# Kernel optimization log

Hardware: AMD Instinct MI355X
Metric: run time of the kernel (lower is better)

Reference implementation:

```python
import jax, jax.numpy as jnp
import numpy as np

HIDDEN = 2048
NUM_HEADS = 16
HEAD_DIM = HIDDEN // NUM_HEADS


def setup_inputs() -> dict:
    key = jax.random.key(0)
    k1, k2, k3 = jax.random.split(key, 3)
    B, S = 2, 2048
    hidden_states = jax.random.normal(k1, (B, S, HIDDEN), dtype=jnp.float32)
    attention_mask = jnp.zeros((B, 1, 1, S), dtype=jnp.float32)
    W_qkv = jax.random.normal(k2, (HIDDEN, 3 * HIDDEN), dtype=jnp.float32) * (1.0 / np.sqrt(HIDDEN))
    b_qkv = jnp.zeros((3 * HIDDEN,), dtype=jnp.float32)
    W_out = jax.random.normal(k3, (HIDDEN, HIDDEN), dtype=jnp.float32) * (1.0 / np.sqrt(HIDDEN))
    b_out = jnp.zeros((HIDDEN,), dtype=jnp.float32)
    return {"hidden_states": hidden_states, "attention_mask": attention_mask,
            "W_qkv": W_qkv, "b_qkv": b_qkv, "W_out": W_out, "b_out": b_out}


def reference(hidden_states, attention_mask, W_qkv, b_qkv, W_out, b_out):
    B, S, H = hidden_states.shape
    scale = 1.0 / np.sqrt(HEAD_DIM)
    # fused QKV projection (column-parallel linear, world_size=1)
    mixed = hidden_states @ W_qkv + b_qkv                      # [B,S,3H]
    q, k, v = jnp.split(mixed, 3, axis=-1)
    # [B, heads, S, head_dim]
    q = q.reshape(B, S, NUM_HEADS, HEAD_DIM).transpose(0, 2, 1, 3)
    k = k.reshape(B, S, NUM_HEADS, HEAD_DIM).transpose(0, 2, 1, 3)
    v = v.reshape(B, S, NUM_HEADS, HEAD_DIM).transpose(0, 2, 1, 3)
    scores = jnp.einsum('bhqd,bhkd->bhqk', q, k) * scale       # [B,h,S,S]
    scores = scores + attention_mask                            # additive mask broadcast
    probs = jax.nn.softmax(scores, axis=-1)
    ctx = jnp.einsum('bhqk,bhkd->bhqd', probs, v)               # [B,h,S,d]
    ctx = ctx.transpose(0, 2, 1, 3).reshape(B, S, H)
    return ctx @ W_out + b_out
```

## Files before the change

kernel.cpp:

```cpp
#include <hip/hip_runtime.h>
#include <hip/hip_bf16.h>
#include <stdint.h>

typedef __attribute__((ext_vector_type(4))) float   f32x4;
typedef __attribute__((ext_vector_type(8))) __bf16  bf16x8;
typedef __attribute__((ext_vector_type(4))) __bf16  bf16x4;
typedef __attribute__((ext_vector_type(8))) short   s16x8;
typedef __attribute__((ext_vector_type(4))) unsigned short u16x4;
typedef __attribute__((ext_vector_type(4))) float   fl4;

#define DEVFN static __device__ __forceinline__

constexpr int BATCH = 2, SEQ = 2048, HID = 2048, NHEAD = 16, HDIM = 128;
constexpr int MROWS = BATCH * SEQ;
constexpr int N3    = 3 * HID;
constexpr float LOG2E = 1.44269504088896340736f;
constexpr float SCALE_LOG2E = 0.12751649736170852f;
constexpr float DEFER_THR = 11.541560327111708f;

DEVFN unsigned short f2bf(float f) {
  unsigned int u = __float_as_uint(f);
  u += 0x7FFFu + ((u >> 16) & 1u);
  return (unsigned short)(u >> 16);
}
DEVFN float bf2f(unsigned short h) { return __uint_as_float(((unsigned int)h) << 16); }

DEVFN void async_cp16(const void* g, void* l) {
  __builtin_amdgcn_global_load_lds(
      (__attribute__((address_space(1))) void*)g,
      (__attribute__((address_space(3))) void*)l, 16, 0, 0);
}

DEVFN f32x4 mfma_bf16(bf16x8 a, bf16x8 b, f32x4 c) {
  return __builtin_amdgcn_mfma_f32_16x16x32_bf16(a, b, c, 0, 0, 0);
}

__global__ __launch_bounds__(256) void cvt_bf16(const float* __restrict__ x,
                                                unsigned short* __restrict__ hi, int n4) {
  for (int i = blockIdx.x * blockDim.x + threadIdx.x; i < n4; i += gridDim.x * blockDim.x) {
    fl4 v = ((const fl4*)x)[i];
    u16x4 h;
#pragma unroll
    for (int j = 0; j < 4; j++) h[j] = f2bf(v[j]);
    ((u16x4*)hi)[i] = h;
  }
}

__global__ __launch_bounds__(256) void cvt_transpose(const float* __restrict__ W,
                                                     unsigned short* __restrict__ T,
                                                     int R, int C) {
  __shared__ float tile[32][33];
  const int c0 = blockIdx.x * 32, r0 = blockIdx.y * 32;
  const int tx = threadIdx.x, ty = threadIdx.y;
#pragma unroll
  for (int i = 0; i < 4; i++) tile[ty + 8 * i][tx] = W[(size_t)(r0 + ty + 8 * i) * C + c0 + tx];
  __syncthreads();
#pragma unroll
  for (int i = 0; i < 4; i++) {
    const float v = tile[tx][ty + 8 * i];
    T[(size_t)(c0 + ty + 8 * i) * R + r0 + tx] = f2bf(v);
  }
}

template <bool OUT_BF16>
__global__ __launch_bounds__(512, 1) void gemm_ring(const unsigned short* __restrict__ A,
                                                    const unsigned short* __restrict__ Bt,
                                                    const float* __restrict__ bias,
                                                    void* __restrict__ Cout, int Ndim) {
  constexpr int KDIM  = 2048;
  constexpr int NT    = KDIM / 64;
  constexpr int ASLOT = 256 * 64;
  constexpr int BSLOT = 128 * 64;
  constexpr int SLOT  = ASLOT + BSLOT;
  __shared__ __align__(16) unsigned short smem[3 * SLOT];

  const int tid = threadIdx.x;
  const int wid = tid >> 6, lane = tid & 63;
  const int wm = wid >> 2, wn = wid & 3;
  const int g = lane >> 4, q = lane & 15;
  const int n0 = blockIdx.x * 128, m0 = blockIdx.y * 256;

  const int srow = (wid << 3) + (lane >> 3);
  const int scol = (((lane & 7) ^ (lane >> 3)) << 4);
  const char* gA = (const char*)A  + ((size_t)(m0 + srow) * KDIM) * 2 + scol;
  const char* gB = (const char*)Bt + ((size_t)(n0 + srow) * KDIM) * 2 + scol;
  const int dbase = ((wid << 3)) << 7;

  f32x4 acc[8][2] = {};
  const int axor = (q & 7) << 4;

  auto STAGE = [&](int tt, int slot) {
    char* sA = (char*)(smem + slot * SLOT);
    char* sB = (char*)(smem + slot * SLOT + ASLOT);
    const size_t koff = (size_t)tt << 7;
#pragma unroll
    for (int i = 0; i < 4; i++)
      async_cp16(gA + (size_t)(i * 64) * (KDIM * 2) + koff, sA + dbase + (i << 13));
#pragma unroll
    for (int i = 0; i < 2; i++)
      async_cp16(gB + (size_t)(i * 64) * (KDIM * 2) + koff, sB + dbase + (i << 13));
  };

  auto COMPUTE = [&](int slot) {
    const char* sA = (const char*)(smem + slot * SLOT);
    const char* sB = (const char*)(smem + slot * SLOT + ASLOT);
#pragma unroll
    for (int ks = 0; ks < 2; ks++) {
      const int kb = (ks << 6) + (g << 4);
      bf16x8 av[8], bv[2];
#pragma unroll
      for (int nf = 0; nf < 2; nf++) {
        const int row = (wn << 5) + (nf << 4) + q;
        bv[nf] = *(const bf16x8*)(sB + (row << 7) + (kb ^ axor));
      }
#pragma unroll
      for (int mf = 0; mf < 8; mf++) {
        const int row = (wm << 7) + (mf << 4) + q;
        av[mf] = *(const bf16x8*)(sA + (row << 7) + (kb ^ axor));
      }
#pragma unroll
      for (int mf = 0; mf < 8; mf++)
#pragma unroll
        for (int nf = 0; nf < 2; nf++)
          acc[mf][nf] = mfma_bf16(av[mf], bv[nf], acc[mf][nf]);
    }
  };

  STAGE(0, 0);
  STAGE(1, 1);
  int s2 = 2, sc = 0;
#pragma unroll 1
  for (int t = 0; t < NT - 2; ++t) {
    asm volatile("s_waitcnt vmcnt(6)" ::: "memory");
    __builtin_amdgcn_s_barrier();
    asm volatile("" ::: "memory");
    STAGE(t + 2, s2);
    COMPUTE(sc);
    s2 = (s2 == 2) ? 0 : s2 + 1;
    sc = (sc == 2) ? 0 : sc + 1;
  }
  asm volatile("s_waitcnt vmcnt(6)" ::: "memory");
  __builtin_amdgcn_s_barrier();
  asm volatile("" ::: "memory");
  COMPUTE(sc);
  sc = (sc == 2) ? 0 : sc + 1;
  asm volatile("s_waitcnt vmcnt(0)" ::: "memory");
  __builtin_amdgcn_s_barrier();
  asm volatile("" ::: "memory");
  COMPUTE(sc);

  float bvv[2];
#pragma unroll
  for (int nf = 0; nf < 2; nf++) bvv[nf] = bias[n0 + (wn << 5) + (nf << 4) + q];
#pragma unroll
  for (int mf = 0; mf < 8; mf++) {
    const int rowg = m0 + (wm << 7) + (mf << 4) + (g << 2);
#pragma unroll
    for (int nf = 0; nf < 2; nf++) {
      const int colg = n0 + (wn << 5) + (nf << 4) + q;
#pragma unroll
      for (int r = 0; r < 4; r++) {
        const float v = acc[mf][nf][r] + bvv[nf];
        if (OUT_BF16)
          ((unsigned short*)Cout)[(size_t)(rowg + r) * Ndim + colg] = f2bf(v);
        else
          ((float*)Cout)[(size_t)(rowg + r) * Ndim + colg] = v;
      }
    }
  }
}

__global__ __launch_bounds__(256) void transpose_v(const unsigned short* __restrict__ qkv,
                                                   unsigned short* __restrict__ vt) {
  __shared__ __align__(16) unsigned short tile[64][136];
  const int z = blockIdx.y, b = z >> 4, h = z & 15;
  const int s0 = blockIdx.x << 6;
  const int t = threadIdx.x;
#pragma unroll
  for (int i = 0; i < 4; i++) {
    const int idx = t + (i << 8);
    const int row = idx >> 4, ch = idx & 15;
    *(s16x8*)&tile[row][ch << 3] =
        *(const s16x8*)(qkv + (size_t)(b * SEQ + s0 + row) * N3 + 2 * HID + h * HDIM + (ch << 3));
  }
  __syncthreads();
#pragma unroll
  for (int i = 0; i < 4; i++) {
    const int idx = t + (i << 8);
    const int d = idx >> 3, sc = idx & 7;
    s16x8 v;
#pragma unroll
    for (int j = 0; j < 8; j++) v[j] = (short)tile[(sc << 3) + j][d];
    *(s16x8*)(vt + (size_t)(z * HDIM + d) * SEQ + s0 + (sc << 3)) = v;
  }
}

__global__ __launch_bounds__(512, 2) void attn_kernel(const unsigned short* __restrict__ qkv,
                                                      const unsigned short* __restrict__ vt,
                                                      const float* __restrict__ mask,
                                                      unsigned short* __restrict__ ctx) {
  constexpr int NT    = SEQ / 64;
  constexpr int KSLOT = 64 * 128;
  constexpr int VSLOT = 128 * 64;
  constexpr int SLOT  = KSLOT + VSLOT;
  __shared__ __align__(16) unsigned short sKV[3 * SLOT];
  __shared__ __align__(16) unsigned short sP[8][32 * 72];
  __shared__ __align__(16) float sM[SEQ];

  const int bid = blockIdx.x;
  const int z  = ((bid & 7) << 2) + ((bid >> 3) >> 3);
  const int qb = (bid >> 3) & 7;
  const int b = z >> 4, h = z & 15;
  const int tid = threadIdx.x, wid = tid >> 6, lane = tid & 63;
  const int g = lane >> 4, q = lane & 15;
  const int q0 = (qb << 8) + (wid << 5);

  {
    fl4 m = ((const fl4*)(mask + (size_t)b * SEQ))[tid];
    m *= LOG2E;
    ((fl4*)sM)[tid] = m;
  }

  bf16x8 bq[2][4];
#pragma unroll
  for (int qs = 0; qs < 2; qs++) {
    const unsigned short* qrow = qkv + (size_t)(b * SEQ + q0 + (qs << 4) + q) * N3 + h * HDIM;
#pragma unroll
    for (int c = 0; c < 4; c++) bq[qs][c] = *(const bf16x8*)(qrow + (c << 5) + (g << 3));
  }

  f32x4 acc[2][8] = {};
  float mrun[2] = {-1e30f, -1e30f}, lrun[2] = {0.f, 0.f};
  unsigned short* myP = &sP[wid][0];
  const int sbase = (lane & 48) | (g << 2);

  const char* gK = (const char*)qkv + ((size_t)(b * SEQ) * N3 + HID + h * HDIM) * 2;
  const char* gV = (const char*)vt + ((size_t)z * HDIM * SEQ) * 2;

  auto STAGE = [&](int tt, int slot) {
    char* base = (char*)(sKV + slot * SLOT);
    const int k0 = tt << 6;
#pragma unroll
    for (int i = 0; i < 2; i++) {
      const int krow = (i << 5) + (tid >> 4);
      const int kc = (((tid & 15) << 4)) ^ ((krow & 7) << 4);
      async_cp16(gK + ((size_t)(k0 + krow) * N3) * 2 + kc, base + (i << 13) + (wid << 10));
    }
#pragma unroll
    for (int i = 0; i < 2; i++) {
      const int vrow = (i << 6) + (tid >> 3);
      const int vc = (((tid & 7) << 4)) ^ ((vrow & 7) << 4);
      async_cp16(gV + ((size_t)vrow * SEQ + k0) * 2 + vc,
                 base + (KSLOT * 2) + (i << 13) + (wid << 10));
    }
  };

  auto COMPUTE = [&](int t, int slot) {
    const char* sK = (const char*)(sKV + slot * SLOT);
    const char* sV = (const char*)(sKV + slot * SLOT + KSLOT);
    const int k0 = t << 6;

    f32x4 accs[2][4];
#pragma unroll
    for (int qs = 0; qs < 2; qs++)
#pragma unroll
      for (int kt = 0; kt < 4; kt++) accs[qs][kt] = (f32x4){0.f, 0.f, 0.f, 0.f};
#pragma unroll
    for (int c = 0; c < 4; c++) {
      const int kbyte = (c << 6) + (g << 4);
#pragma unroll
      for (int kt = 0; kt < 4; kt++) {
        const int key = (kt << 4) + q;
        const bf16x8 ak = *(const bf16x8*)(sK + (key << 8) + (kbyte ^ ((key & 7) << 4)));
        accs[0][kt] = mfma_bf16(ak, bq[0][c], accs[0][kt]);
        accs[1][kt] = mfma_bf16(ak, bq[1][c], accs[1][kt]);
      }
    }

    fl4 mk2[4];
#pragma unroll
    for (int kt = 0; kt < 4; kt++) mk2[kt] = *(const fl4*)&sM[k0 + (kt << 4) + (g << 2)];

#pragma unroll
    for (int qs = 0; qs < 2; qs++) {
      float s2[4][4];
      float km[4];
#pragma unroll
      for (int kt = 0; kt < 4; kt++) {
#pragma unroll
        for (int r = 0; r < 4; r++)
          s2[kt][r] = fmaf(accs[qs][kt][r], SCALE_LOG2E, mk2[kt][r]);
        km[kt] = fmaxf(fmaxf(s2[kt][0], s2[kt][1]), fmaxf(s2[kt][2], s2[kt][3]));
      }
      float mt = fmaxf(fmaxf(km[0], km[1]), fmaxf(km[2], km[3]));
      mt = fmaxf(mt, __shfl_xor(mt, 16));
      mt = fmaxf(mt, __shfl_xor(mt, 32));
      if (!__all(mt <= mrun[qs] + DEFER_THR)) {
        const float mnew = fmaxf(mrun[qs], mt);
        const float fs = exp2f(mrun[qs] - mnew);
        lrun[qs] *= fs;
#pragma unroll
        for (int r = 0; r < 4; r++) {
          const float fr = __shfl(fs, sbase + r);
#pragma unroll
          for (int dt = 0; dt < 8; dt++) acc[qs][dt][r] *= fr;
        }
        mrun[qs] = mnew;
      }
      float pst[4];
#pragma unroll
      for (int kt = 0; kt < 4; kt++) {
        bf16x4 pk;
        float e0 = exp2f(s2[kt][0] - mrun[qs]);
        float e1 = exp2f(s2[kt][1] - mrun[qs]);
        float e2 = exp2f(s2[kt][2] - mrun[qs]);
        float e3 = exp2f(s2[kt][3] - mrun[qs]);
        pk[0] = (__bf16)e0; pk[1] = (__bf16)e1; pk[2] = (__bf16)e2; pk[3] = (__bf16)e3;
        pst[kt] = (e0 + e1) + (e2 + e3);
        *(bf16x4*)((char*)myP + ((qs << 4) + q) * 144 + (((kt << 4) + (g << 2)) << 1)) = pk;
      }
      float ps = (pst[0] + pst[1]) + (pst[2] + pst[3]);
      ps += __shfl_xor(ps, 16);
      ps += __shfl_xor(ps, 32);
      lrun[qs] += ps;
    }

    asm volatile("s_waitcnt lgkmcnt(0)" ::: "memory");
    __builtin_amdgcn_sched_barrier(0);

#pragma unroll
    for (int kc = 0; kc < 2; kc++) {
      const bf16x8 pa0 = *(const bf16x8*)((const char*)myP + q * 144 + (kc << 6) + (g << 4));
      const bf16x8 pa1 = *(const bf16x8*)((const char*)myP + (16 + q) * 144 + (kc << 6) + (g << 4));
      const int kbyte = (kc << 6) + (g << 4);
#pragma unroll
      for (int dt = 0; dt < 8; dt++) {
        const int d = (dt << 4) + q;
        const bf16x8 bvv = *(const bf16x8*)(sV + (d << 7) + (kbyte ^ ((d & 7) << 4)));
        acc[0][dt] = mfma_bf16(pa0, bvv, acc[0][dt]);
        acc[1][dt] = mfma_bf16(pa1, bvv, acc[1][dt]);
      }
    }
  };

  STAGE(0, 0);
  STAGE(1, 1);
  __syncthreads();
  int s2 = 2, sc = 0;
#pragma unroll 1
  for (int t = 0; t < NT - 2; ++t) {
    asm volatile("s_waitcnt vmcnt(4)" ::: "memory");
    __builtin_amdgcn_s_barrier();
    asm volatile("" ::: "memory");
    STAGE(t + 2, s2);
    COMPUTE(t, sc);
    s2 = (s2 == 2) ? 0 : s2 + 1;
    sc = (sc == 2) ? 0 : sc + 1;
  }
  asm volatile("s_waitcnt vmcnt(4)" ::: "memory");
  __builtin_amdgcn_s_barrier();
  asm volatile("" ::: "memory");
  COMPUTE(NT - 2, sc);
  sc = (sc == 2) ? 0 : sc + 1;
  asm volatile("s_waitcnt vmcnt(0)" ::: "memory");
  __builtin_amdgcn_s_barrier();
  asm volatile("" ::: "memory");
  COMPUTE(NT - 1, sc);

#pragma unroll
  for (int qs = 0; qs < 2; qs++)
#pragma unroll
    for (int r = 0; r < 4; r++) {
      const float lr = __shfl(lrun[qs], sbase + r);
      const float inv = 1.f / lr;
      const int token = b * SEQ + q0 + (qs << 4) + (g << 2) + r;
      unsigned short* crow = ctx + (size_t)token * HID + h * HDIM + q;
#pragma unroll
      for (int dt = 0; dt < 8; dt++) crow[dt << 4] = f2bf(acc[qs][dt][r] * inv);
    }
}

extern "C" void kernel_launch(void* const* d_in, const int* in_sizes, int n_in,
                              void* d_out, int out_size, void* d_ws, size_t ws_size,
                              hipStream_t stream) {
  const float* hs   = (const float*)d_in[0];
  const float* mask = (const float*)d_in[1];
  const float* Wqkv = (const float*)d_in[2];
  const float* bqkv = (const float*)d_in[3];
  const float* Wout = (const float*)d_in[4];
  const float* bout = (const float*)d_in[5];

  char* ws = (char*)d_ws;
  size_t off = 0;
  auto alloc = [&](size_t n) { char* p = ws + off; off += (n + 255) & ~(size_t)255; return p; };
  unsigned short* hs_bf = (unsigned short*)alloc((size_t)MROWS * HID * 2);
  unsigned short* wq_bf = (unsigned short*)alloc((size_t)N3 * HID * 2);
  unsigned short* wo_bf = (unsigned short*)alloc((size_t)HID * HID * 2);
  unsigned short* qkvb  = (unsigned short*)alloc((size_t)MROWS * N3 * 2);
  unsigned short* vtb   = (unsigned short*)alloc((size_t)BATCH * NHEAD * HDIM * SEQ * 2);
  unsigned short* ctxb  = (unsigned short*)alloc((size_t)MROWS * HID * 2);
  (void)ws_size;

  cvt_bf16<<<2048, 256, 0, stream>>>(hs, hs_bf, MROWS * HID / 4);
  dim3 tb(32, 8);
  cvt_transpose<<<dim3(N3 / 32, HID / 32), tb, 0, stream>>>(Wqkv, wq_bf, HID, N3);
  cvt_transpose<<<dim3(HID / 32, HID / 32), tb, 0, stream>>>(Wout, wo_bf, HID, HID);
  gemm_ring<true ><<<dim3(N3 / 128, MROWS / 256), 512, 0, stream>>>(hs_bf, wq_bf, bqkv, qkvb, N3);
  transpose_v<<<dim3(SEQ / 64, BATCH * NHEAD), 256, 0, stream>>>(qkvb, vtb);
  attn_kernel<<<256, 512, 0, stream>>>(qkvb, vtb, mask, ctxb);
  gemm_ring<false><<<dim3(HID / 128, MROWS / 256), 512, 0, stream>>>(ctxb, wo_bf, bout, (float*)d_out, HID);
}
```

Measured before the change: 272.6 us.

## Switch attention to 32x32x16 MFMA with in-register P via permlane32 swap

Rewrites the attention inner loop to use 32x32x16 bf16 MFMA tiles, so each wave computes S^T for 32 queries by 32 keys and accumulates the output with 32-wide tiles. The probability matrix is packed with v_cvt_pk_bf16 and rearranged across lane halves using permlane32_swap, which removes the per-wave shared-memory P buffer and its LDS round trip and wait. It also raises wave priority around the MFMA blocks. This reduces LDS traffic and instruction count, at the cost of a more intricate register layout and possible register pressure at two waves per SIMD.

Result: no change. 268.9 us (-1.3%).

```diff
diff --git a/kernel.cpp b/kernel.cpp
--- a/kernel.cpp
+++ b/kernel.cpp
@@ -2,12 +2,14 @@
 #include <hip/hip_bf16.h>
 #include <stdint.h>
 
-typedef __attribute__((ext_vector_type(4))) float   f32x4;
-typedef __attribute__((ext_vector_type(8))) __bf16  bf16x8;
-typedef __attribute__((ext_vector_type(4))) __bf16  bf16x4;
-typedef __attribute__((ext_vector_type(8))) short   s16x8;
-typedef __attribute__((ext_vector_type(4))) unsigned short u16x4;
-typedef __attribute__((ext_vector_type(4))) float   fl4;
+typedef __attribute__((ext_vector_type(4)))  float   f32x4;
+typedef __attribute__((ext_vector_type(16))) float   f32x16;
+typedef __attribute__((ext_vector_type(8)))  __bf16  bf16x8;
+typedef __attribute__((ext_vector_type(8)))  short   s16x8;
+typedef __attribute__((ext_vector_type(4)))  unsigned short u16x4;
+typedef __attribute__((ext_vector_type(4)))  float   fl4;
+typedef __attribute__((ext_vector_type(2)))  unsigned int u32x2;
+typedef __attribute__((ext_vector_type(4)))  unsigned int u32x4;
 
 #define DEVFN static __device__ __forceinline__
 
@@ -33,6 +35,14 @@
 
 DEVFN f32x4 mfma_bf16(bf16x8 a, bf16x8 b, f32x4 c) {
   return __builtin_amdgcn_mfma_f32_16x16x32_bf16(a, b, c, 0, 0, 0);
+}
+DEVFN f32x16 mfma32(bf16x8 a, bf16x8 b, f32x16 c) {
+  return __builtin_amdgcn_mfma_f32_32x32x16_bf16(a, b, c, 0, 0, 0);
+}
+DEVFN unsigned cvt_pk_bf16(float lo, float hi) {
+  unsigned r;
+  asm("v_cvt_pk_bf16_f32 %0, %1, %2" : "=v"(r) : "v"(lo), "v"(hi));
+  return r;
 }
 
 __global__ __launch_bounds__(256) void cvt_bf16(const float* __restrict__ x,
@@ -204,7 +214,6 @@
   constexpr int VSLOT = 128 * 64;
   constexpr int SLOT  = KSLOT + VSLOT;
   __shared__ __align__(16) unsigned short sKV[3 * SLOT];
-  __shared__ __align__(16) unsigned short sP[8][32 * 72];
   __shared__ __align__(16) float sM[SEQ];
 
   const int bid = blockIdx.x;
@@ -212,8 +221,8 @@
   const int qb = (bid >> 3) & 7;
   const int b = z >> 4, h = z & 15;
   const int tid = threadIdx.x, wid = tid >> 6, lane = tid & 63;
-  const int g = lane >> 4, q = lane & 15;
-  const int q0 = (qb << 8) + (wid << 5);
+  const int l31 = lane & 31, hi = lane >> 5;
+  const int q0w = (qb << 8) + (wid << 5);
 
   {
     fl4 m = ((const fl4*)(mask + (size_t)b * SEQ))[tid];
@@ -221,18 +230,15 @@
     ((fl4*)sM)[tid] = m;
   }
 
-  bf16x8 bq[2][4];
-#pragma unroll
-  for (int qs = 0; qs < 2; qs++) {
-    const unsigned short* qrow = qkv + (size_t)(b * SEQ + q0 + (qs << 4) + q) * N3 + h * HDIM;
-#pragma unroll
-    for (int c = 0; c < 4; c++) bq[qs][c] = *(const bf16x8*)(qrow + (c << 5) + (g << 3));
-  }
-
-  f32x4 acc[2][8] = {};
-  float mrun[2] = {-1e30f, -1e30f}, lrun[2] = {0.f, 0.f};
-  unsigned short* myP = &sP[wid][0];
-  const int sbase = (lane & 48) | (g << 2);
+  bf16x8 bq[8];
+  {
+    const char* qrow = (const char*)(qkv + (size_t)(b * SEQ + q0w + l31) * N3 + h * HDIM);
+#pragma unroll
+    for (int kc = 0; kc < 8; kc++) bq[kc] = *(const bf16x8*)(qrow + (kc << 5) + (hi << 4));
+  }
+
+  f32x16 acc2[4] = {};
+  float mrun = -1e30f, lrun = 0.f;
 
   const char* gK = (const char*)qkv + ((size_t)(b * SEQ) * N3 + HID + h * HDIM) * 2;
   const char* gV = (const char*)vt + ((size_t)z * HDIM * SEQ) * 2;
@@ -260,87 +266,85 @@
     const char* sV = (const char*)(sKV + slot * SLOT + KSLOT);
     const int k0 = t << 6;
 
-    f32x4 accs[2][4];
-#pragma unroll
-    for (int qs = 0; qs < 2; qs++)
-#pragma unroll
-      for (int kt = 0; kt < 4; kt++) accs[qs][kt] = (f32x4){0.f, 0.f, 0.f, 0.f};
-#pragma unroll
-    for (int c = 0; c < 4; c++) {
-      const int kbyte = (c << 6) + (g << 4);
-#pragma unroll
-      for (int kt = 0; kt < 4; kt++) {
-        const int key = (kt << 4) + q;
-        const bf16x8 ak = *(const bf16x8*)(sK + (key << 8) + (kbyte ^ ((key & 7) << 4)));
-        accs[0][kt] = mfma_bf16(ak, bq[0][c], accs[0][kt]);
-        accs[1][kt] = mfma_bf16(ak, bq[1][c], accs[1][kt]);
-      }
-    }
-
-    fl4 mk2[4];
-#pragma unroll
-    for (int kt = 0; kt < 4; kt++) mk2[kt] = *(const fl4*)&sM[k0 + (kt << 4) + (g << 2)];
-
-#pragma unroll
-    for (int qs = 0; qs < 2; qs++) {
-      float s2[4][4];
-      float km[4];
-#pragma unroll
-      for (int kt = 0; kt < 4; kt++) {
-#pragma unroll
-        for (int r = 0; r < 4; r++)
-          s2[kt][r] = fmaf(accs[qs][kt][r], SCALE_LOG2E, mk2[kt][r]);
-        km[kt] = fmaxf(fmaxf(s2[kt][0], s2[kt][1]), fmaxf(s2[kt][2], s2[kt][3]));
-      }
-      float mt = fmaxf(fmaxf(km[0], km[1]), fmaxf(km[2], km[3]));
-      mt = fmaxf(mt, __shfl_xor(mt, 16));
-      mt = fmaxf(mt, __shfl_xor(mt, 32));
-      if (!__all(mt <= mrun[qs] + DEFER_THR)) {
-        const float mnew = fmaxf(mrun[qs], mt);
-        const float fs = exp2f(mrun[qs] - mnew);
-        lrun[qs] *= fs;
-#pragma unroll
-        for (int r = 0; r < 4; r++) {
-          const float fr = __shfl(fs, sbase + r);
-#pragma unroll
-          for (int dt = 0; dt < 8; dt++) acc[qs][dt][r] *= fr;
-        }
-        mrun[qs] = mnew;
-      }
-      float pst[4];
-#pragma unroll
-      for (int kt = 0; kt < 4; kt++) {
-        bf16x4 pk;
-        float e0 = exp2f(s2[kt][0] - mrun[qs]);
-        float e1 = exp2f(s2[kt][1] - mrun[qs]);
-        float e2 = exp2f(s2[kt][2] - mrun[qs]);
-        float e3 = exp2f(s2[kt][3] - mrun[qs]);
-        pk[0] = (__bf16)e0; pk[1] = (__bf16)e1; pk[2] = (__bf16)e2; pk[3] = (__bf16)e3;
-        pst[kt] = (e0 + e1) + (e2 + e3);
-        *(bf16x4*)((char*)myP + ((qs << 4) + q) * 144 + (((kt << 4) + (g << 2)) << 1)) = pk;
-      }
-      float ps = (pst[0] + pst[1]) + (pst[2] + pst[3]);
-      ps += __shfl_xor(ps, 16);
-      ps += __shfl_xor(ps, 32);
-      lrun[qs] += ps;
-    }
-
-    asm volatile("s_waitcnt lgkmcnt(0)" ::: "memory");
-    __builtin_amdgcn_sched_barrier(0);
-
-#pragma unroll
-    for (int kc = 0; kc < 2; kc++) {
-      const bf16x8 pa0 = *(const bf16x8*)((const char*)myP + q * 144 + (kc << 6) + (g << 4));
-      const bf16x8 pa1 = *(const bf16x8*)((const char*)myP + (16 + q) * 144 + (kc << 6) + (g << 4));
-      const int kbyte = (kc << 6) + (g << 4);
-#pragma unroll
-      for (int dt = 0; dt < 8; dt++) {
-        const int d = (dt << 4) + q;
-        const bf16x8 bvv = *(const bf16x8*)(sV + (d << 7) + (kbyte ^ ((d & 7) << 4)));
-        acc[0][dt] = mfma_bf16(pa0, bvv, acc[0][dt]);
-        acc[1][dt] = mfma_bf16(pa1, bvv, acc[1][dt]);
-      }
-    }
+    f32x16 accs[2] = {};
+    __builtin_amdgcn_s_setprio(1);
+#pragma unroll
+    for (int kb = 0; kb < 2; kb++)
+#pragma unroll
+      for (int kc = 0; kc < 8; kc++) {
+        const bf16x8 ka = *(const bf16x8*)(sK + (((kb << 5) + l31) << 8) +
+                                           (((kc << 5) + (hi << 4)) ^ ((l31 & 7) << 4)));
+        accs[kb] = mfma32(ka, bq[kc], accs[kb]);
+      }
+    __builtin_amdgcn_s_setprio(0);
+
+    float p_[2][16];
+#pragma unroll
+    for (int kb = 0; kb < 2; kb++) {
+      fl4 mk[4];
+#pragma unroll
+      for (int m = 0; m < 4; m++) mk[m] = *(const fl4*)&sM[k0 + (kb << 5) + (m << 3) + (hi << 2)];
+#pragma unroll
+      for (int r = 0; r < 16; r++)
+        p_[kb][r] = fmaf(accs[kb][r], SCALE_LOG2E, mk[r >> 2][r & 3]);
+    }
+    float mt = p_[0][0];
+#pragma unroll
+    for (int kb = 0; kb < 2; kb++)
+#pragma unroll
+      for (int r = 0; r < 16; r++) mt = fmaxf(mt, p_[kb][r]);
+    mt = fmaxf(mt, __shfl_xor(mt, 32));
+    if (!__all(mt <= mrun + DEFER_THR)) {
+      const float mnew = fmaxf(mrun, mt);
+      const float fs = exp2f(mrun - mnew);
+      lrun *= fs;
+#pragma unroll
+      for (int r = 0; r < 16; r++) {
+        const int qr = (r & 3) + ((r >> 2) << 3) + (hi << 2);
+        const float fr = __shfl(fs, (lane & 32) | qr);
+#pragma unroll
+        for (int db = 0; db < 4; db++) acc2[db][r] *= fr;
+      }
+      mrun = mnew;
+    }
+    float ps = 0.f;
+#pragma unroll
+    for (int kb = 0; kb < 2; kb++)
+#pragma unroll
+      for (int r = 0; r < 16; r++) {
+        const float e = exp2f(p_[kb][r] - mrun);
+        p_[kb][r] = e;
+        ps += e;
+      }
+    ps += __shfl_xor(ps, 32);
+    lrun += ps;
+
+    bf16x8 pa[4];
+#pragma unroll
+    for (int kb = 0; kb < 2; kb++)
+#pragma unroll
+      for (int hh = 0; hh < 2; hh++) {
+        const float* pp = &p_[kb][hh << 3];
+        const unsigned x01 = cvt_pk_bf16(pp[0], pp[1]);
+        const unsigned x23 = cvt_pk_bf16(pp[2], pp[3]);
+        const unsigned y01 = cvt_pk_bf16(pp[4], pp[5]);
+        const unsigned y23 = cvt_pk_bf16(pp[6], pp[7]);
+        const u32x2 sa = __builtin_amdgcn_permlane32_swap(x01, y01, false, false);
+        const u32x2 sb = __builtin_amdgcn_permlane32_swap(x23, y23, false, false);
+        const u32x4 w = {sa[0], sb[0], sa[1], sb[1]};
+        pa[(kb << 1) + hh] = __builtin_bit_cast(bf16x8, w);
+      }
+
+    __builtin_amdgcn_s_setprio(1);
+#pragma unroll
+    for (int db = 0; db < 4; db++)
+#pragma unroll
+      for (int ks = 0; ks < 4; ks++) {
+        const bf16x8 bv = *(const bf16x8*)(sV + (((db << 5) + l31) << 7) +
+                                           (((ks << 5) + (hi << 4)) ^ ((l31 & 7) << 4)));
+        acc2[db] = mfma32(pa[ks], bv, acc2[db]);
+      }
+    __builtin_amdgcn_s_setprio(0);
   };
 
   STAGE(0, 0);
@@ -367,17 +371,15 @@
   asm volatile("" ::: "memory");
   COMPUTE(NT - 1, sc);
 
-#pragma unroll
-  for (int qs = 0; qs < 2; qs++)
-#pragma unroll
-    for (int r = 0; r < 4; r++) {
-      const float lr = __shfl(lrun[qs], sbase + r);
-      const float inv = 1.f / lr;
-      const int token = b * SEQ + q0 + (qs << 4) + (g << 2) + r;
-      unsigned short* crow = ctx + (size_t)token * HID + h * HDIM + q;
-#pragma unroll
-      for (int dt = 0; dt < 8; dt++) crow[dt << 4] = f2bf(acc[qs][dt][r] * inv);
-    }
+  const float inv = 1.f / lrun;
+#pragma unroll
+  for (int r = 0; r < 16; r++) {
+    const int qr = (r & 3) + ((r >> 2) << 3) + (hi << 2);
+    const float fr = __shfl(inv, (lane & 32) | qr);
+    unsigned short* crow = ctx + (size_t)(b * SEQ + q0w + qr) * HID + h * HDIM + l31;
+#pragma unroll
+    for (int db = 0; db < 4; db++) crow[db << 5] = f2bf(acc2[db][r] * fr);
+  }
 }
 
 extern "C" void kernel_launch(void* const* d_in, const int* in_sizes, int n_in,
```
